# Optimization experiments

Measured on AMD Instinct MI355X. Metric: run time of the kernel, lower is better.

The kernel has to match this reference:

```python
import jax, jax.numpy as jnp
import numpy as np

INV_PI = 0.31830988618
PI_over_2 = 1.57079632679
PI_over_4 = 0.78539816339
N_MODES, DIM, COND_C = 8, 2, 64
LAYERS = [COND_C, 128, 512, 128, 32, N_MODES * DIM * 2 + N_MODES + 1]
N = 262144


def setup_inputs() -> dict:
    key = jax.random.key(0)
    ks = jax.random.split(key, 2 + 2 * (len(LAYERS) - 1))
    inp = {}
    inp["cond_vec"] = jax.random.normal(ks[0], (N, COND_C), jnp.float32)
    # uniforms in (0,1), bounded away from 0/1 so log/div are finite
    inp["randseed"] = jax.random.uniform(ks[1], (N, 2), jnp.float32, 1e-4, 1.0 - 1e-4)
    for i in range(len(LAYERS) - 1):
        inp[f"W{i}"] = jax.random.normal(ks[2 + 2 * i], (LAYERS[i], LAYERS[i + 1]), jnp.float32) * 0.01
        inp[f"b{i}"] = jnp.zeros((LAYERS[i + 1],), jnp.float32)
    return inp


def _mlp(x, Ws, bs):
    for i, (W, b) in enumerate(zip(Ws, bs)):
        x = x @ W + b
        if i < len(Ws) - 1:
            x = jax.nn.relu(x)
    return x


def _forward(cond_vec, randseed, Ws, bs):
    nm, d = N_MODES, DIM
    h = _mlp(cond_vec, Ws, bs)  # [N, nm*d*2 + nm + 1]
    loc = h[:, : nm * d].reshape(-1, nm, d)
    log_scale = h[:, nm * d : 2 * nm * d].reshape(-1, nm, d)
    w = jnp.abs(h[:, 2 * nm * d :])
    w = w / jnp.sum(w, axis=1, keepdims=True)  # [N, nm+1]
    wL = w[:, -1]

    r0, r1 = randseed[:, 0], randseed[:, 1]
    lambert_mask = r0 < wL
    gauss_mask = ~lambert_mask
    # in-place rescale of randseed column 0 in the torch code
    u0 = jnp.where(lambert_mask, r0 / wL, (r0 - wL) / (1.0 - wL))

    # --- gauss branch (Box-Muller) ---
    U1 = jnp.where(gauss_mask, u0, 0.5)  # masked positions: safe dummy
    U1 = jnp.maximum(U1, 1e-12)
    R = jnp.sqrt(-2.0 * jnp.log(U1))
    th = 2.0 * jnp.pi * r1
    eps_ = jnp.stack([R * jnp.cos(th), R * jnp.sin(th)], axis=-1)  # [N, 2]
    scale_sample = jnp.sum(jnp.exp(log_scale), axis=1)  # [N, 2]
    loc_sample = jnp.sum(loc, axis=1)  # [N, 2]
    z_gauss = eps_ * scale_sample + loc_sample

    # --- lambert branch (concentric disk map) ---
    wo0 = u0 * 2.0 - 1.0
    wo1 = r1 * 2.0 - 1.0
    nonzero = ~((wo0 == 0) & (wo1 == 0))
    cond1 = (jnp.abs(wo0) > jnp.abs(wo1)) & nonzero
    cond2 = (~cond1) & nonzero
    safe0 = jnp.where(wo0 == 0, 1.0, wo0)
    safe1 = jnp.where(wo1 == 0, 1.0, wo1)
    phi = jnp.where(cond1, PI_over_4 * wo1 / safe0, PI_over_2 - PI_over_4 * wo0 / safe1)
    r = jnp.where(cond1, wo0, jnp.where(cond2, wo1, 0.0))
    z_lambert = jnp.stack([r * jnp.cos(phi), r * jnp.sin(phi)], axis=-1)

    z = jnp.where(lambert_mask[:, None], z_lambert, z_gauss)  # [N, 2]

    # --- mixture log prob ---
    eps = (z[:, None, :] - loc) / jnp.exp(log_scale)  # [N, nm, 2]
    log_p = (-0.5 * d * jnp.log(2.0 * jnp.pi)
             + jnp.log(w[:, :-1] + 1e-5)
             - 0.5 * jnp.sum(eps ** 2, axis=2)
             - jnp.sum(log_scale, axis=2))  # [N, nm]
    pdf = jnp.where(z[:, 0] ** 2 + z[:, 1] ** 2 > 1.0, 0.0, INV_PI)
    lambert_log_p = jnp.log(pdf + 1e-5) + jnp.log(wL)
    log_p = jnp.concatenate([log_p, lambert_log_p[:, None]], axis=-1)  # [N, nm+1]
    return z, jax.scipy.special.logsumexp(log_p, axis=1)


def reference(cond_vec, randseed, W0, b0, W1, b1, W2, b2, W3, b3, W4, b4):
    Ws = [W0, W1, W2, W3, W4]
    bs = [b0, b1, b2, b3, b4]
    return _forward(cond_vec, randseed, Ws, bs)
```

## Files before the change

### kernel.cpp

```cpp
#include <hip/hip_runtime.h>
#include <math.h>

#define NTOT 262144
#define BROWS 32
#define THREADS 256
#define PITCH 140

typedef short bf16x8 __attribute__((ext_vector_type(8)));
typedef float f32x16 __attribute__((ext_vector_type(16)));

#define O0H 0
#define O0L 8192
#define O1H 16384
#define O1L 81920
#define O2H 147456
#define O2L 212992
#define GCNT_OFF 557056
#define GLIST_OFF 557120

#define SOFTBAR() asm volatile("s_waitcnt lgkmcnt(0)\n\ts_barrier" ::: "memory")
#define WAITV(N) do{ asm volatile("s_waitcnt vmcnt(" #N ")" ::: "memory"); \
                     __builtin_amdgcn_sched_barrier(0); }while(0)
#define LOADG4(r0, r1, r2, r3, base) do{ \
    asm volatile("global_load_dwordx4 %0, %1, %2 offset:0"    : "=v"(r0) : "v"(voff), "s"(base)); \
    asm volatile("global_load_dwordx4 %0, %1, %2 offset:1024" : "=v"(r1) : "v"(voff), "s"(base)); \
    asm volatile("global_load_dwordx4 %0, %1, %2 offset:2048" : "=v"(r2) : "v"(voff), "s"(base)); \
    asm volatile("global_load_dwordx4 %0, %1, %2 offset:3072" : "=v"(r3) : "v"(voff), "s"(base)); \
}while(0)

__device__ __forceinline__ unsigned short bf16_rne(float x){
    unsigned u = __float_as_uint(x);
    return (unsigned short)((u + 0x7FFFu + ((u >> 16) & 1u)) >> 16);
}
__device__ __forceinline__ void split2(float x, unsigned short& h, unsigned short& l){
    h = bf16_rne(x);
    float xh = __uint_as_float(((unsigned)h) << 16);
    l = bf16_rne(x - xh);
}

__device__ __forceinline__ int frag_off(int n, int k, int nks){
    return ((((n >> 5) * nks + (k >> 4)) << 9) | (((k >> 3) & 1) << 8) | ((n & 31) << 3) | (k & 7));
}

__global__ void prep_weights(const float* __restrict__ W0, const float* __restrict__ W1,
                             const float* __restrict__ W2, unsigned short* __restrict__ ws){
    int i = blockIdx.x * 256 + threadIdx.x;
    float v; int oh, ol;
    if (i < 8192){
        int n = i >> 6, k = i & 63; v = W0[k*128 + n];
        int o = frag_off(n, k, 4);  oh = O0H + o; ol = O0L + o;
    } else if (i < 73728){
        int j = i - 8192; int n = j >> 7, k = j & 127; v = W1[k*512 + n];
        int o = frag_off(n, k, 8);  oh = O1H + o; ol = O1L + o;
    } else if (i < 139264){
        int j = i - 73728; int n = j >> 9, k = j & 511; v = W2[k*128 + n];
        int o = frag_off(n, k, 32); oh = O2H + o; ol = O2L + o;
    } else return;
    unsigned short h, l; split2(v, h, l);
    ws[oh] = h; ws[ol] = l;
}

__device__ __forceinline__ void epilogue_row(const float* __restrict__ h, float r0v, float r1v,
        float& z0o, float& z1o, float& lseo, float& wLo, float& u0o, bool& lamo){
    float wraw[9]; float wsum = 0.0f;
    #pragma unroll
    for (int j = 0; j < 9; ++j){ wraw[j] = fabsf(h[32 + j]); wsum += wraw[j]; }
    float wL = wraw[8] / wsum;
    const bool lambert = r0v < wL;
    float u0 = lambert ? (r0v / wL) : ((r0v - wL) / (1.0f - wL));
    float U1 = lambert ? 0.5f : u0;
    U1 = fmaxf(U1, 1e-12f);
    float R  = sqrtf(-2.0f * logf(U1));
    float th = 6.28318530717958647692f * r1v;
    float ce = cosf(th), se = sinf(th);
    float es0[8], es1[8];
    float ssum0 = 0.0f, ssum1 = 0.0f, lsum0 = 0.0f, lsum1 = 0.0f;
    #pragma unroll
    for (int m = 0; m < 8; ++m){
        es0[m] = expf(h[16 + 2*m]); es1[m] = expf(h[16 + 2*m + 1]);
        ssum0 += es0[m]; ssum1 += es1[m];
        lsum0 += h[2*m]; lsum1 += h[2*m + 1];
    }
    float zg0 = (R * ce) * ssum0 + lsum0;
    float zg1 = (R * se) * ssum1 + lsum1;
    float wo0 = u0 * 2.0f - 1.0f;
    float wo1 = r1v * 2.0f - 1.0f;
    bool nonzero = !((wo0 == 0.0f) && (wo1 == 0.0f));
    bool c1 = (fabsf(wo0) > fabsf(wo1)) && nonzero;
    bool c2 = (!c1) && nonzero;
    float sa0 = (wo0 == 0.0f) ? 1.0f : wo0;
    float sa1 = (wo1 == 0.0f) ? 1.0f : wo1;
    float phi = c1 ? (0.78539816339f * wo1 / sa0)
                   : (1.57079632679f - 0.78539816339f * wo0 / sa1);
    float rr = c1 ? wo0 : (c2 ? wo1 : 0.0f);
    float zl0 = rr * cosf(phi);
    float zl1 = rr * sinf(phi);
    float z0 = lambert ? zl0 : zg0;
    float z1 = lambert ? zl1 : zg1;
    float lp[9];
    #pragma unroll
    for (int m = 0; m < 8; ++m){
        float e0 = (z0 - h[2*m])     / es0[m];
        float e1 = (z1 - h[2*m + 1]) / es1[m];
        float wm = wraw[m] / wsum;
        lp[m] = (-1.83787706640934548356f + logf(wm + 1e-5f))
                - 0.5f * (e0*e0 + e1*e1)
                - (h[16 + 2*m] + h[16 + 2*m + 1]);
    }
    float pdf = (z0*z0 + z1*z1 > 1.0f) ? 0.0f : 0.31830988618f;
    lp[8] = logf(pdf + 1e-5f) + logf(wL);
    float mx = lp[0];
    #pragma unroll
    for (int j = 1; j < 9; ++j) mx = fmaxf(mx, lp[j]);
    float s = 0.0f;
    #pragma unroll
    for (int j = 0; j < 9; ++j) s += expf(lp[j] - mx);
    z0o = z0; z1o = z1; lseo = mx + logf(s); wLo = wL; u0o = u0; lamo = lambert;
}

__device__ __forceinline__ bool flag_row(float r0v, float z0, float z1, float wL, float u0, bool lam){
    return (fabsf(r0v - wL) < 5e-3f)
        || (wL < 3e-3f) || (wL > 0.5f)
        || (fabsf(z0*z0 + z1*z1 - 1.0f) < (lam ? 0.02f : 0.2f))
        || (!lam && u0 < 3e-3f);
}

__device__ __forceinline__ f32x16 bias_init(const float* __restrict__ b, int mt, int lane, int nmax){
    f32x16 c;
    const int hq = ((lane >> 5) << 2);
    #pragma unroll
    for (int r = 0; r < 16; ++r){
        int n = mt + (r & 3) + ((r >> 2) << 3) + hq;
        c[r] = (n < nmax) ? b[n] : 0.0f;
    }
    return c;
}

__device__ __forceinline__ void write_tile(unsigned short* __restrict__ ah, unsigned short* __restrict__ al,
        int brow, int m0, int lane, const f32x16 acc, bool relu){
    const int hq = ((lane >> 5) << 2);
    #pragma unroll
    for (int q = 0; q < 4; ++q){
        ushort4 vh, vl;
        #pragma unroll
        for (int r = 0; r < 4; ++r){
            float x = acc[q*4 + r];
            if (relu) x = fmaxf(x, 0.0f);
            unsigned short hh, ll; split2(x, hh, ll);
            (&vh.x)[r] = hh; (&vl.x)[r] = ll;
        }
        const int off = brow*PITCH + m0 + q*8 + hq;
        *(ushort4*)(ah + off) = vh;
        *(ushort4*)(al + off) = vl;
    }
}

__device__ __forceinline__ void write_tile_f32t(float* __restrict__ dst,
        int brow, int m0, int lane, const f32x16 acc){
    const int hq = ((lane >> 5) << 2);
    #pragma unroll
    for (int q = 0; q < 4; ++q){
        #pragma unroll
        for (int r = 0; r < 4; ++r){
            int n = m0 + q*8 + hq + r;
            dst[n*32 + brow] = fmaxf(acc[q*4 + r], 0.0f);
        }
    }
}

__device__ __forceinline__ void mfma_half(const bf16x8* wh, const bf16x8* wl,
        const unsigned short* __restrict__ acth, const unsigned short* __restrict__ actl,
        int ks0, int brow, int lane, f32x16& acc){
    const int kl = ((lane >> 5) << 3);
    __builtin_amdgcn_s_setprio(1);
    #pragma unroll
    for (int i = 0; i < 4; ++i){
        const int k0 = (ks0 + i)*16 + kl;
        bf16x8 ah = *(const bf16x8*)(acth + brow*PITCH + k0);
        bf16x8 al = *(const bf16x8*)(actl + brow*PITCH + k0);
        acc = __builtin_amdgcn_mfma_f32_32x32x16_bf16(wh[i], ah, acc, 0, 0, 0);
        acc = __builtin_amdgcn_mfma_f32_32x32x16_bf16(wh[i], al, acc, 0, 0, 0);
        acc = __builtin_amdgcn_mfma_f32_32x32x16_bf16(wl[i], ah, acc, 0, 0, 0);
    }
    __builtin_amdgcn_s_setprio(0);
}

__global__ __launch_bounds__(THREADS, 4)
void gmm_mfma(const float* __restrict__ cond, const float* __restrict__ rnd,
              const unsigned short* __restrict__ ws,
              const float* __restrict__ b0, const float* __restrict__ b1,
              const float* __restrict__ b2,
              const float* __restrict__ W3, const float* __restrict__ b3,
              const float* __restrict__ W4, const float* __restrict__ b4,
              int* __restrict__ gcnt, int* __restrict__ glist,
              float* __restrict__ out)
{
    extern __shared__ unsigned char smem[];
    unsigned short* aAh = (unsigned short*)smem;
    unsigned short* aAl = aAh + 32*PITCH;
    unsigned short* aBh = (unsigned short*)(smem + 17920);
    unsigned short* aBl = aBh + 32*PITCH;
    float* h2f = (float*)smem;
    float* h3f = (float*)(smem + 17920);
    float* h4f = (float*)(smem + 22016);
    float* b1g = (float*)(smem + 35840);
    float* b2g = b1g + 512;

    const int tid  = threadIdx.x;
    const int lane = tid & 63;
    const int wv   = tid >> 6;
    const int row0 = blockIdx.x * BROWS;
    const int ct   = wv;
    const int brow = lane & 31;
    const int m0   = ct * 32;
    const int kl   = ((lane >> 5) << 3);
    const unsigned voff = (unsigned)lane * 16;

    bf16x8 whA[4], wlA[4], whB[4], wlB[4];

    b1g[tid] = b1[tid];
    b1g[tid + 256] = b1[tid + 256];
    if (tid < 128) b2g[tid] = b2[tid];

    {
        f32x16 acc0 = bias_init(b0, m0, lane, 128);
        #pragma unroll 2
        for (int ks = 0; ks < 4; ++ks){
            const int k0 = ks*16 + kl;
            const float* cp = cond + (size_t)(row0 + brow)*64 + k0;
            float4 ca = *(const float4*)cp;
            float4 cb = *(const float4*)(cp + 4);
            float xs[8] = {ca.x, ca.y, ca.z, ca.w, cb.x, cb.y, cb.z, cb.w};
            bf16x8 ah, al;
            #pragma unroll
            for (int j = 0; j < 8; ++j){
                unsigned short hh, ll; split2(xs[j], hh, ll);
                ah[j] = (short)hh; al[j] = (short)ll;
            }
            bf16x8 wh = *(const bf16x8*)(ws + O0H + (ct*4 + ks)*512 + lane*8);
            bf16x8 wl = *(const bf16x8*)(ws + O0L + (ct*4 + ks)*512 + lane*8);
            acc0 = __builtin_amdgcn_mfma_f32_32x32x16_bf16(wh, ah, acc0, 0, 0, 0);
            acc0 = __builtin_amdgcn_mfma_f32_32x32x16_bf16(wh, al, acc0, 0, 0, 0);
            acc0 = __builtin_amdgcn_mfma_f32_32x32x16_bf16(wl, ah, acc0, 0, 0, 0);
        }
        write_tile(aAh, aAl, brow, m0, lane, acc0, true);
    }

    asm volatile("s_waitcnt vmcnt(0)" ::: "memory");
    __builtin_amdgcn_sched_barrier(0);
    {
        const unsigned short* p1h = ws + O1H + __builtin_amdgcn_readfirstlane(ct*4096);
        const unsigned short* p1l = ws + O1L + __builtin_amdgcn_readfirstlane(ct*4096);
        LOADG4(whA[0], whA[1], whA[2], whA[3], p1h);
        LOADG4(wlA[0], wlA[1], wlA[2], wlA[3], p1l);
    }
    SOFTBAR();

    f32x16 acc2 = bias_init(b2g, m0, lane, 128);
    #pragma unroll
    for (int c = 0; c < 4; ++c){
        const unsigned short* b1h = ws + O1H + __builtin_amdgcn_readfirstlane((c*4 + ct)*4096);
        const unsigned short* b1l = ws + O1L + __builtin_amdgcn_readfirstlane((c*4 + ct)*4096);
        const unsigned short* c2h = ws + O2H + __builtin_amdgcn_readfirstlane((ct*32 + c*8)*512);
        const unsigned short* c2l = ws + O2L + __builtin_amdgcn_readfirstlane((ct*32 + c*8)*512);

        LOADG4(whB[0], whB[1], whB[2], whB[3], b1h + 2048);
        LOADG4(wlB[0], wlB[1], wlB[2], wlB[3], b1l + 2048);
        WAITV(8);
        f32x16 a1 = bias_init(b1g + c*128, m0, lane, 128);
        mfma_half(whA, wlA, aAh, aAl, 0, brow, lane, a1);

        LOADG4(whA[0], whA[1], whA[2], whA[3], c2h);
        LOADG4(wlA[0], wlA[1], wlA[2], wlA[3], c2l);
        WAITV(8);
        mfma_half(whB, wlB, aAh, aAl, 4, brow, lane, a1);

        LOADG4(whB[0], whB[1], whB[2], whB[3], c2h + 2048);
        LOADG4(wlB[0], wlB[1], wlB[2], wlB[3], c2l + 2048);
        SOFTBAR();
        write_tile(aBh, aBl, brow, m0, lane, a1, true);
        SOFTBAR();
        WAITV(8);
        mfma_half(whA, wlA, aBh, aBl, 0, brow, lane, acc2);

        if (c < 3){
            const unsigned short* n1h = ws + O1H + __builtin_amdgcn_readfirstlane(((c+1)*4 + ct)*4096);
            const unsigned short* n1l = ws + O1L + __builtin_amdgcn_readfirstlane(((c+1)*4 + ct)*4096);
            LOADG4(whA[0], whA[1], whA[2], whA[3], n1h);
            LOADG4(wlA[0], wlA[1], wlA[2], wlA[3], n1l);
            WAITV(8);
        } else {
            WAITV(0);
        }
        mfma_half(whB, wlB, aBh, aBl, 4, brow, lane, acc2);
    }
    write_tile_f32t(h2f, brow, m0, lane, acc2);
    SOFTBAR();

    {
        const int row = tid & 31;
        const int nb  = tid >> 5;
        float acc[4];
        #pragma unroll
        for (int c = 0; c < 4; ++c) acc[c] = b3[nb*4 + c];
        #pragma unroll 8
        for (int k = 0; k < 128; ++k){
            float a = h2f[k*32 + row];
            const float* wr = W3 + k*32 + nb*4;
            #pragma unroll
            for (int c = 0; c < 4; ++c) acc[c] = fmaf(a, wr[c], acc[c]);
        }
        SOFTBAR();
        #pragma unroll
        for (int c = 0; c < 4; ++c) h3f[(nb*4 + c)*32 + row] = fmaxf(acc[c], 0.0f);
    }
    SOFTBAR();

    {
        const int row = tid & 31;
        const int nb  = tid >> 5;
        float acc[6];
        #pragma unroll
        for (int c = 0; c < 6; ++c){ int n = nb*6 + c; acc[c] = (n < 41) ? b4[n] : 0.0f; }
        #pragma unroll 8
        for (int k = 0; k < 32; ++k){
            float a = h3f[k*32 + row];
            const float* wr = W4 + k*41;
            #pragma unroll
            for (int c = 0; c < 6; ++c){ int n = nb*6 + c; if (n < 41) acc[c] = fmaf(a, wr[n], acc[c]); }
        }
        #pragma unroll
        for (int c = 0; c < 6; ++c){ int n = nb*6 + c; if (n < 41) h4f[n*32 + row] = acc[c]; }
    }
    SOFTBAR();

    if (tid < 32){
        const int row  = tid;
        const int grow = row0 + row;
        float h[41];
        #pragma unroll
        for (int j = 0; j < 41; ++j) h[j] = h4f[j*32 + row];
        float2 rv = *(const float2*)(rnd + 2*(size_t)grow);
        float z0, z1, lse, wL, u0; bool lam;
        epilogue_row(h, rv.x, rv.y, z0, z1, lse, wL, u0, lam);
        ((float2*)out)[grow] = make_float2(z0, z1);
        out[(size_t)2*NTOT + grow] = lse;
        if (flag_row(rv.x, z0, z1, wL, u0, lam)){
            int idx = atomicAdd(gcnt, 1); glist[idx] = grow;
        }
    }
}

__global__ __launch_bounds__(512, 2)
void gmm_fix(const float* __restrict__ cond, const float* __restrict__ rnd,
             const float* __restrict__ W0, const float* __restrict__ b0,
             const float* __restrict__ W1, const float* __restrict__ b1,
             const float* __restrict__ W2, const float* __restrict__ b2,
             const float* __restrict__ W3, const float* __restrict__ b3,
             const float* __restrict__ W4, const float* __restrict__ b4,
             const int* __restrict__ gcnt, const int* __restrict__ glist,
             float* __restrict__ out)
{
    __shared__ float fb[7296];
    float* c0g = fb;
    float* f0g = fb + 512;
    float* f1g = fb + 1536;
    float* f2g = fb + 5632;
    float* f3g = fb + 6656;
    float* h4g = fb + 6912;
    const int tid = threadIdx.x;
    const int nflag = *gcnt;

    for (int base = blockIdx.x * 8; base < nflag; base += gridDim.x * 8){
        const int g = min(8, nflag - base);
        {
            int i = tid >> 6, k = tid & 63;
            if (i < g) c0g[i*64 + k] = cond[(size_t)glist[base + i]*64 + k];
        }
        __syncthreads();
        if (tid < 128){
            float acc[8];
            #pragma unroll
            for (int i = 0; i < 8; ++i) acc[i] = b0[tid];
            #pragma unroll 8
            for (int k = 0; k < 64; ++k){
                float w = W0[k*128 + tid];
                #pragma unroll
                for (int i = 0; i < 8; ++i) acc[i] = fmaf(c0g[i*64 + k], w, acc[i]);
            }
            for (int i = 0; i < g; ++i) f0g[i*128 + tid] = fmaxf(acc[i], 0.0f);
        }
        __syncthreads();
        {
            float acc[8];
            #pragma unroll
            for (int i = 0; i < 8; ++i) acc[i] = b1[tid];
            #pragma unroll 8
            for (int k = 0; k < 128; ++k){
                float w = W1[k*512 + tid];
                #pragma unroll
                for (int i = 0; i < 8; ++i) acc[i] = fmaf(f0g[i*128 + k], w, acc[i]);
            }
            for (int i = 0; i < g; ++i) f1g[i*512 + tid] = fmaxf(acc[i], 0.0f);
        }
        __syncthreads();
        if (tid < 128){
            float acc[8];
            #pragma unroll
            for (int i = 0; i < 8; ++i) acc[i] = b2[tid];
            #pragma unroll 8
            for (int k = 0; k < 512; ++k){
                float w = W2[k*128 + tid];
                #pragma unroll
                for (int i = 0; i < 8; ++i) acc[i] = fmaf(f1g[i*512 + k], w, acc[i]);
            }
            for (int i = 0; i < g; ++i) f2g[i*128 + tid] = fmaxf(acc[i], 0.0f);
        }
        __syncthreads();
        if (tid < 32){
            float acc[8];
            #pragma unroll
            for (int i = 0; i < 8; ++i) acc[i] = b3[tid];
            #pragma unroll 8
            for (int k = 0; k < 128; ++k){
                float w = W3[k*32 + tid];
                #pragma unroll
                for (int i = 0; i < 8; ++i) acc[i] = fmaf(f2g[i*128 + k], w, acc[i]);
            }
            for (int i = 0; i < g; ++i) f3g[i*32 + tid] = fmaxf(acc[i], 0.0f);
        }
        __syncthreads();
        if (tid < 41){
            float acc[8];
            #pragma unroll
            for (int i = 0; i < 8; ++i) acc[i] = b4[tid];
            #pragma unroll 8
            for (int k = 0; k < 32; ++k){
                float w = W4[k*41 + tid];
                #pragma unroll
                for (int i = 0; i < 8; ++i) acc[i] = fmaf(f3g[i*32 + k], w, acc[i]);
            }
            for (int i = 0; i < g; ++i) h4g[i*48 + tid] = acc[i];
        }
        __syncthreads();
        if (tid < g){
            const int grow = glist[base + tid];
            float2 rv = *(const float2*)(rnd + 2*(size_t)grow);
            float z0, z1, lse, wL, u0; bool lam;
            epilogue_row(&h4g[tid*48], rv.x, rv.y, z0, z1, lse, wL, u0, lam);
            ((float2*)out)[grow] = make_float2(z0, z1);
            out[(size_t)2*NTOT + grow] = lse;
        }
        __syncthreads();
    }
}

extern "C" void kernel_launch(void* const* d_in, const int* in_sizes, int n_in,
                              void* d_out, int out_size, void* d_ws, size_t ws_size,
                              hipStream_t stream) {
    const float* cond = (const float*)d_in[0];
    const float* rnd  = (const float*)d_in[1];
    const float* W0 = (const float*)d_in[2];  const float* b0 = (const float*)d_in[3];
    const float* W1 = (const float*)d_in[4];  const float* b1 = (const float*)d_in[5];
    const float* W2 = (const float*)d_in[6];  const float* b2 = (const float*)d_in[7];
    const float* W3 = (const float*)d_in[8];  const float* b3 = (const float*)d_in[9];
    const float* W4 = (const float*)d_in[10]; const float* b4 = (const float*)d_in[11];
    float* out = (float*)d_out;
    unsigned short* ws = (unsigned short*)d_ws;
    int* gcnt  = (int*)((char*)d_ws + GCNT_OFF);
    int* glist = (int*)((char*)d_ws + GLIST_OFF);

    hipMemsetAsync(gcnt, 0, 4, stream);
    hipLaunchKernelGGL(prep_weights, dim3(544), dim3(256), 0, stream, W0, W1, W2, ws);

    hipLaunchKernelGGL(gmm_mfma, dim3(NTOT / BROWS), dim3(THREADS), 38400, stream,
                       cond, rnd, ws, b0, b1, b2, W3, b3, W4, b4, gcnt, glist, out);

    hipLaunchKernelGGL(gmm_fix, dim3(1024), dim3(512), 0, stream,
                       cond, rnd, W0, b0, W1, b1, W2, b2, W3, b3, W4, b4, gcnt, glist, out);
}
```

Measured before the change: 804.0 us.

## Keep layer-1 output in registers and split layer-2 K across waves

Layer 1 and 2 are restructured so each wave computes its own 128-wide slice of the 512 hidden units. It converts them to bf16 hi/lo in registers via permlane32 swaps and feeds them straight into partial layer-2 MFMAs for all four output tiles. The partial sums are then reduced across waves through LDS. This removes the LDS round-trip for the layer-1 activations, the per-chunk barriers and the explicit global prefetch pipeline. In exchange it holds four accumulator tiles per wave, which lowers the occupancy bound from 4 to 3, and it adds a larger LDS reduction buffer.

```diff
diff --git a/kernel.cpp b/kernel.cpp
--- a/kernel.cpp
+++ b/kernel.cpp
@@ -4,10 +4,11 @@
 #define NTOT 262144
 #define BROWS 32
 #define THREADS 256
-#define PITCH 140
+#define PITCH 132
 
 typedef short bf16x8 __attribute__((ext_vector_type(8)));
 typedef float f32x16 __attribute__((ext_vector_type(16)));
+typedef int   i32x4  __attribute__((ext_vector_type(4)));
 
 #define O0H 0
 #define O0L 8192
@@ -19,14 +20,6 @@
 #define GLIST_OFF 557120
 
 #define SOFTBAR() asm volatile("s_waitcnt lgkmcnt(0)\n\ts_barrier" ::: "memory")
-#define WAITV(N) do{ asm volatile("s_waitcnt vmcnt(" #N ")" ::: "memory"); \
-                     __builtin_amdgcn_sched_barrier(0); }while(0)
-#define LOADG4(r0, r1, r2, r3, base) do{ \
-    asm volatile("global_load_dwordx4 %0, %1, %2 offset:0"    : "=v"(r0) : "v"(voff), "s"(base)); \
-    asm volatile("global_load_dwordx4 %0, %1, %2 offset:1024" : "=v"(r1) : "v"(voff), "s"(base)); \
-    asm volatile("global_load_dwordx4 %0, %1, %2 offset:2048" : "=v"(r2) : "v"(voff), "s"(base)); \
-    asm volatile("global_load_dwordx4 %0, %1, %2 offset:3072" : "=v"(r3) : "v"(voff), "s"(base)); \
-}while(0)
 
 __device__ __forceinline__ unsigned short bf16_rne(float x){
     unsigned u = __float_as_uint(x);
@@ -168,24 +161,7 @@
     }
 }
 
-__device__ __forceinline__ void mfma_half(const bf16x8* wh, const bf16x8* wl,
-        const unsigned short* __restrict__ acth, const unsigned short* __restrict__ actl,
-        int ks0, int brow, int lane, f32x16& acc){
-    const int kl = ((lane >> 5) << 3);
-    __builtin_amdgcn_s_setprio(1);
-    #pragma unroll
-    for (int i = 0; i < 4; ++i){
-        const int k0 = (ks0 + i)*16 + kl;
-        bf16x8 ah = *(const bf16x8*)(acth + brow*PITCH + k0);
-        bf16x8 al = *(const bf16x8*)(actl + brow*PITCH + k0);
-        acc = __builtin_amdgcn_mfma_f32_32x32x16_bf16(wh[i], ah, acc, 0, 0, 0);
-        acc = __builtin_amdgcn_mfma_f32_32x32x16_bf16(wh[i], al, acc, 0, 0, 0);
-        acc = __builtin_amdgcn_mfma_f32_32x32x16_bf16(wl[i], ah, acc, 0, 0, 0);
-    }
-    __builtin_amdgcn_s_setprio(0);
-}
-
-__global__ __launch_bounds__(THREADS, 4)
+__global__ __launch_bounds__(THREADS, 3)
 void gmm_mfma(const float* __restrict__ cond, const float* __restrict__ rnd,
               const unsigned short* __restrict__ ws,
               const float* __restrict__ b0, const float* __restrict__ b1,
@@ -198,13 +174,10 @@
     extern __shared__ unsigned char smem[];
     unsigned short* aAh = (unsigned short*)smem;
     unsigned short* aAl = aAh + 32*PITCH;
-    unsigned short* aBh = (unsigned short*)(smem + 17920);
-    unsigned short* aBl = aBh + 32*PITCH;
+    float* red = (float*)smem;
     float* h2f = (float*)smem;
-    float* h3f = (float*)(smem + 17920);
-    float* h4f = (float*)(smem + 22016);
-    float* b1g = (float*)(smem + 35840);
-    float* b2g = b1g + 512;
+    float* h3f = (float*)(smem + 16384);
+    float* h4f = (float*)(smem + 20480);
 
     const int tid  = threadIdx.x;
     const int lane = tid & 63;
@@ -214,13 +187,6 @@
     const int brow = lane & 31;
     const int m0   = ct * 32;
     const int kl   = ((lane >> 5) << 3);
-    const unsigned voff = (unsigned)lane * 16;
-
-    bf16x8 whA[4], wlA[4], whB[4], wlB[4];
-
-    b1g[tid] = b1[tid];
-    b1g[tid + 256] = b1[tid + 256];
-    if (tid < 128) b2g[tid] = b2[tid];
 
     {
         f32x16 acc0 = bias_init(b0, m0, lane, 128);
@@ -245,56 +211,88 @@
         }
         write_tile(aAh, aAl, brow, m0, lane, acc0, true);
     }
-
-    asm volatile("s_waitcnt vmcnt(0)" ::: "memory");
-    __builtin_amdgcn_sched_barrier(0);
-    {
-        const unsigned short* p1h = ws + O1H + __builtin_amdgcn_readfirstlane(ct*4096);
-        const unsigned short* p1l = ws + O1L + __builtin_amdgcn_readfirstlane(ct*4096);
-        LOADG4(whA[0], whA[1], whA[2], whA[3], p1h);
-        LOADG4(wlA[0], wlA[1], wlA[2], wlA[3], p1l);
-    }
-    SOFTBAR();
-
-    f32x16 acc2 = bias_init(b2g, m0, lane, 128);
-    #pragma unroll
-    for (int c = 0; c < 4; ++c){
-        const unsigned short* b1h = ws + O1H + __builtin_amdgcn_readfirstlane((c*4 + ct)*4096);
-        const unsigned short* b1l = ws + O1L + __builtin_amdgcn_readfirstlane((c*4 + ct)*4096);
-        const unsigned short* c2h = ws + O2H + __builtin_amdgcn_readfirstlane((ct*32 + c*8)*512);
-        const unsigned short* c2l = ws + O2L + __builtin_amdgcn_readfirstlane((ct*32 + c*8)*512);
-
-        LOADG4(whB[0], whB[1], whB[2], whB[3], b1h + 2048);
-        LOADG4(wlB[0], wlB[1], wlB[2], wlB[3], b1l + 2048);
-        WAITV(8);
-        f32x16 a1 = bias_init(b1g + c*128, m0, lane, 128);
-        mfma_half(whA, wlA, aAh, aAl, 0, brow, lane, a1);
-
-        LOADG4(whA[0], whA[1], whA[2], whA[3], c2h);
-        LOADG4(wlA[0], wlA[1], wlA[2], wlA[3], c2l);
-        WAITV(8);
-        mfma_half(whB, wlB, aAh, aAl, 4, brow, lane, a1);
-
-        LOADG4(whB[0], whB[1], whB[2], whB[3], c2h + 2048);
-        LOADG4(wlB[0], wlB[1], wlB[2], wlB[3], c2l + 2048);
-        SOFTBAR();
-        write_tile(aBh, aBl, brow, m0, lane, a1, true);
-        SOFTBAR();
-        WAITV(8);
-        mfma_half(whA, wlA, aBh, aBl, 0, brow, lane, acc2);
-
-        if (c < 3){
-            const unsigned short* n1h = ws + O1H + __builtin_amdgcn_readfirstlane(((c+1)*4 + ct)*4096);
-            const unsigned short* n1l = ws + O1L + __builtin_amdgcn_readfirstlane(((c+1)*4 + ct)*4096);
-            LOADG4(whA[0], whA[1], whA[2], whA[3], n1h);
-            LOADG4(wlA[0], wlA[1], wlA[2], wlA[3], n1l);
-            WAITV(8);
+    SOFTBAR();
+
+    f32x16 acc2p[4];
+    #pragma unroll
+    for (int t = 0; t < 4; ++t){
+        if (t == ct){
+            acc2p[t] = bias_init(b2, t*32, lane, 128);
         } else {
-            WAITV(0);
-        }
-        mfma_half(whB, wlB, aBh, aBl, 4, brow, lane, acc2);
-    }
-    write_tile_f32t(h2f, brow, m0, lane, acc2);
+            #pragma unroll
+            for (int r = 0; r < 16; ++r) acc2p[t][r] = 0.0f;
+        }
+    }
+
+    #pragma unroll 1
+    for (int sub = 0; sub < 4; ++sub){
+        f32x16 a1 = bias_init(b1, ct*128 + sub*32, lane, 512);
+        const int wb1 = ((ct*4 + sub)*8)*512;
+        #pragma unroll
+        for (int ks = 0; ks < 8; ++ks){
+            const int k0 = ks*16 + kl;
+            bf16x8 ah = *(const bf16x8*)(aAh + brow*PITCH + k0);
+            bf16x8 al = *(const bf16x8*)(aAl + brow*PITCH + k0);
+            bf16x8 wh = *(const bf16x8*)(ws + O1H + wb1 + ks*512 + lane*8);
+            bf16x8 wl = *(const bf16x8*)(ws + O1L + wb1 + ks*512 + lane*8);
+            a1 = __builtin_amdgcn_mfma_f32_32x32x16_bf16(wh, ah, a1, 0, 0, 0);
+            a1 = __builtin_amdgcn_mfma_f32_32x32x16_bf16(wh, al, a1, 0, 0, 0);
+            a1 = __builtin_amdgcn_mfma_f32_32x32x16_bf16(wl, ah, a1, 0, 0, 0);
+        }
+        unsigned Ph[8], Pl[8];
+        #pragma unroll
+        for (int p = 0; p < 8; ++p){
+            float x0 = fmaxf(a1[2*p], 0.0f), x1 = fmaxf(a1[2*p+1], 0.0f);
+            unsigned short h0_, l0_, h1_, l1_;
+            split2(x0, h0_, l0_); split2(x1, h1_, l1_);
+            Ph[p] = (unsigned)h0_ | ((unsigned)h1_ << 16);
+            Pl[p] = (unsigned)l0_ | ((unsigned)l1_ << 16);
+        }
+        #pragma unroll
+        for (int ks2 = 0; ks2 < 2; ++ks2){
+            unsigned hw0 = Ph[ks2*4+0], hw2 = Ph[ks2*4+2];
+            unsigned hw1 = Ph[ks2*4+1], hw3 = Ph[ks2*4+3];
+            unsigned lw0 = Pl[ks2*4+0], lw2 = Pl[ks2*4+2];
+            unsigned lw1 = Pl[ks2*4+1], lw3 = Pl[ks2*4+3];
+            asm volatile("v_permlane32_swap_b32 %0, %1" : "+v"(hw0), "+v"(hw2));
+            asm volatile("v_permlane32_swap_b32 %0, %1" : "+v"(hw1), "+v"(hw3));
+            asm volatile("v_permlane32_swap_b32 %0, %1" : "+v"(lw0), "+v"(lw2));
+            asm volatile("v_permlane32_swap_b32 %0, %1" : "+v"(lw1), "+v"(lw3));
+            i32x4 bhv = { (int)hw0, (int)hw1, (int)hw2, (int)hw3 };
+            i32x4 blv = { (int)lw0, (int)lw1, (int)lw2, (int)lw3 };
+            bf16x8 Bh = *(bf16x8*)&bhv;
+            bf16x8 Bl = *(bf16x8*)&blv;
+            const int kb = ct*8 + sub*2 + ks2;
+            #pragma unroll
+            for (int t = 0; t < 4; ++t){
+                bf16x8 w2h = *(const bf16x8*)(ws + O2H + (t*32 + kb)*512 + lane*8);
+                bf16x8 w2l = *(const bf16x8*)(ws + O2L + (t*32 + kb)*512 + lane*8);
+                acc2p[t] = __builtin_amdgcn_mfma_f32_32x32x16_bf16(w2h, Bh, acc2p[t], 0, 0, 0);
+                acc2p[t] = __builtin_amdgcn_mfma_f32_32x32x16_bf16(w2h, Bl, acc2p[t], 0, 0, 0);
+                acc2p[t] = __builtin_amdgcn_mfma_f32_32x32x16_bf16(w2l, Bh, acc2p[t], 0, 0, 0);
+            }
+        }
+    }
+
+    SOFTBAR();
+    #pragma unroll
+    for (int t = 0; t < 4; ++t){
+        if (t == ct) continue;
+        const int s = (ct > t) ? (ct - 1) : ct;
+        #pragma unroll
+        for (int r = 0; r < 16; ++r)
+            red[((t*3 + s)*16 + r)*64 + lane] = acc2p[t][r];
+    }
+    SOFTBAR();
+    f32x16 acc2 = acc2p[ct];
+    #pragma unroll
+    for (int s = 0; s < 3; ++s){
+        #pragma unroll
+        for (int r = 0; r < 16; ++r)
+            acc2[r] += red[((ct*3 + s)*16 + r)*64 + lane];
+    }
+    SOFTBAR();
+    write_tile_f32t(h2f, brow, ct*32, lane, acc2);
     SOFTBAR();
 
     {
@@ -470,10 +468,10 @@
     int* gcnt  = (int*)((char*)d_ws + GCNT_OFF);
     int* glist = (int*)((char*)d_ws + GLIST_OFF);
 
-    hipMemsetAsync(gcnt, 0, 4, stream);
+    (void)hipMemsetAsync(gcnt, 0, 4, stream);
     hipLaunchKernelGGL(prep_weights, dim3(544), dim3(256), 0, stream, W0, W1, W2, ws);
 
-    hipLaunchKernelGGL(gmm_mfma, dim3(NTOT / BROWS), dim3(THREADS), 38400, stream,
+    hipLaunchKernelGGL(gmm_mfma, dim3(NTOT / BROWS), dim3(THREADS), 49152, stream,
                        cond, rnd, ws, b0, b1, b2, W3, b3, W4, b4, gcnt, glist, out);
 
     hipLaunchKernelGGL(gmm_fix, dim3(1024), dim3(512), 0, stream,
```

Result: slower. 855.8 us (+6.4%).
